# Performance work log

Hardware: AMD Instinct MI355X
Metric: run time of the kernel (lower is better)

## Reference

```python
import jax, jax.numpy as jnp
import numpy as np

B, S, D_IN = 16, 1024, 1024
H, D_OUT = 16, 128

def setup_inputs() -> dict:
    key = jax.random.key(0)
    k1, k2, k3 = jax.random.split(key, 3)
    x = jax.random.normal(k1, (B, S, D_IN), dtype=jnp.float32)
    W = jax.random.normal(k2, (H, 3, D_IN, D_OUT), dtype=jnp.float32) * (1.0 / np.sqrt(D_IN))
    Wo = jax.random.normal(k3, (H * D_OUT, D_OUT), dtype=jnp.float32) * (1.0 / np.sqrt(H * D_OUT))
    return {"x": x, "W": W, "Wo": Wo}

def reference(x, W, Wo):
    # x: [B,S,D_IN], W: [H,3,D_IN,E], Wo: [H*E,E]
    E = W.shape[-1]
    q = jnp.einsum('bsd,hde->bhse', x, W[:, 0])
    k = jnp.einsum('bsd,hde->bhse', x, W[:, 1])
    v = jnp.einsum('bsd,hde->bhse', x, W[:, 2])
    # NOTE: source divides by (output_dim * 0.5), not sqrt(output_dim)
    scores = jnp.einsum('bhse,bhte->bhst', q, k) / (E * 0.5)
    attn = jax.nn.softmax(scores, axis=-1)
    o = jnp.einsum('bhst,bhte->bhse', attn, v)          # [B,H,S,E]
    o = jnp.transpose(o, (0, 2, 1, 3)).reshape(x.shape[0], x.shape[1], -1)  # concat heads
    return jnp.einsum('bsf,fe->bse', o, Wo)
```

## Files before the change

### kernel.cpp

```cpp
#include <hip/hip_runtime.h>

typedef unsigned short u16;
typedef _Float16 f16;
typedef __attribute__((ext_vector_type(8))) _Float16 half8;
typedef __attribute__((ext_vector_type(4))) _Float16 half4;
typedef __attribute__((ext_vector_type(2))) _Float16 half2v;
typedef __attribute__((ext_vector_type(8))) short short8;
typedef __attribute__((ext_vector_type(4))) float f32x4;
typedef __attribute__((ext_vector_type(4))) float f4;
typedef __attribute__((ext_vector_type(4))) u16 u16x4;

#define B_ 16
#define S_ 1024
#define DIN_ 1024
#define H_ 16
#define E_ 128

#define EXPK 0.0225546041776533f

__device__ __forceinline__ u16 f2h(float f) {
  f16 h = (f16)f;
  return __builtin_bit_cast(u16, h);
}

__device__ __forceinline__ half2v pkrtz(float a, float b) {
  return __builtin_bit_cast(half2v, __builtin_amdgcn_cvt_pkrtz(a, b));
}

__device__ __forceinline__ void gl2lds16(const u16* g, u16* l) {
  __builtin_amdgcn_global_load_lds((const __attribute__((address_space(1))) void*)g,
                                   (__attribute__((address_space(3))) void*)l, 16, 0, 0);
}

__global__ __launch_bounds__(256) void zero_f32(float* __restrict__ p) {
  int i = (blockIdx.x * 256 + threadIdx.x) * 4;
  f4 z = {0.f, 0.f, 0.f, 0.f};
  *reinterpret_cast<f4*>(p + i) = z;
}

__global__ __launch_bounds__(256) void cvt_f32_f16(const float* __restrict__ in,
                                                   u16* __restrict__ out) {
  int i = (blockIdx.x * 256 + threadIdx.x) * 4;
  f4 v = *reinterpret_cast<const f4*>(in + i);
  u16x4 o;
  o[0] = f2h(v[0]); o[1] = f2h(v[1]); o[2] = f2h(v[2]); o[3] = f2h(v[3]);
  *reinterpret_cast<u16x4*>(out + i) = o;
}

__global__ __launch_bounds__(256) void transpose_cvt(const float* __restrict__ in,
                                                     u16* __restrict__ out,
                                                     int R, int C) {
  __shared__ float tile[32][33];
  const size_t moff = (size_t)blockIdx.z * R * C;
  const float* src = in + moff;
  u16* dst = out + moff;
  int c0 = blockIdx.x * 32, r0 = blockIdx.y * 32;
  int tx = threadIdx.x & 31, ty = threadIdx.x >> 5;
#pragma unroll
  for (int i = 0; i < 32; i += 8)
    tile[ty + i][tx] = src[(size_t)(r0 + ty + i) * C + c0 + tx];
  __syncthreads();
#pragma unroll
  for (int i = 0; i < 32; i += 8)
    dst[(size_t)(c0 + ty + i) * R + r0 + tx] = f2h(tile[tx][ty + i]);
}

template<int MODE, int KSPLIT, int K>
__global__ __launch_bounds__(256) void gemm_bt(const u16* __restrict__ A,
                                               const u16* __restrict__ BT,
                                               u16* __restrict__ q, u16* __restrict__ kk,
                                               u16* __restrict__ vT, float* __restrict__ out) {
  const int tid = threadIdx.x;
  const int m0 = blockIdx.x * 128;
  const u16* Bblk = BT + (size_t)blockIdx.y * 128 * K;
  __shared__ __align__(16) u16 smem[132 * 128];
  u16* As = smem;
  u16* Bs = smem + 8192;
  const int w = tid >> 6, lane = tid & 63;
  const int quad = lane >> 4, ln = lane & 15;
  const int wr = w >> 1, wc = w & 1;

  const int kbeg = (KSPLIT > 1) ? blockIdx.z * (K / KSPLIT) : 0;
  constexpr int KLEN = K / KSPLIT;

  const int rr = lane >> 3;
  const int cc = (lane & 7) ^ rr;
  const u16* agp[4];
  const u16* bgp[4];
#pragma unroll
  for (int i = 0; i < 4; i++) {
    int row = i * 32 + w * 8 + rr;
    agp[i] = A + (size_t)(m0 + row) * K + kbeg + cc * 8;
    bgp[i] = Bblk + (size_t)row * K + kbeg + cc * 8;
  }

  int offA[4][2], offB[4][2];
#pragma unroll
  for (int mt = 0; mt < 4; mt++) {
    int row = wr * 64 + mt * 16 + ln;
#pragma unroll
    for (int k2 = 0; k2 < 2; k2++)
      offA[mt][k2] = row * 64 + (((k2 * 4 + quad) ^ (ln & 7)) * 8);
  }
#pragma unroll
  for (int nt = 0; nt < 4; nt++) {
    int row = wc * 64 + nt * 16 + ln;
#pragma unroll
    for (int k2 = 0; k2 < 2; k2++)
      offB[nt][k2] = row * 64 + (((k2 * 4 + quad) ^ (ln & 7)) * 8);
  }

  f32x4 acc[4][4];
  f32x4 zero = {0.f, 0.f, 0.f, 0.f};
#pragma unroll
  for (int mt = 0; mt < 4; mt++)
#pragma unroll
    for (int nt = 0; nt < 4; nt++) acc[mt][nt] = zero;

#pragma unroll
  for (int k0 = 0; k0 < KLEN; k0 += 64) {
    __syncthreads();
#pragma unroll
    for (int i = 0; i < 4; i++) {
      gl2lds16(agp[i] + k0, As + i * 2048 + w * 512);
      gl2lds16(bgp[i] + k0, Bs + i * 2048 + w * 512);
    }
    __syncthreads();
#pragma unroll
    for (int k2 = 0; k2 < 2; k2++) {
      half8 af[4], bfr[4];
#pragma unroll
      for (int mt = 0; mt < 4; mt++)
        af[mt] = *reinterpret_cast<const half8*>(&As[offA[mt][k2]]);
#pragma unroll
      for (int nt = 0; nt < 4; nt++)
        bfr[nt] = *reinterpret_cast<const half8*>(&Bs[offB[nt][k2]]);
#pragma unroll
      for (int mt = 0; mt < 4; mt++)
#pragma unroll
        for (int nt = 0; nt < 4; nt++)
          acc[mt][nt] = __builtin_amdgcn_mfma_f32_16x16x32_f16(af[mt], bfr[nt], acc[mt][nt], 0, 0, 0);
    }
  }

  if (MODE == 0) {
    const int h = blockIdx.y / 3, c = blockIdx.y % 3;
    if (c < 2) {
      u16* dst = (c == 0) ? q : kk;
      const float sc = (c == 0) ? EXPK : 1.0f;
#pragma unroll
      for (int mt = 0; mt < 4; mt++)
#pragma unroll
        for (int nt = 0; nt < 4; nt++)
#pragma unroll
          for (int r = 0; r < 4; r++) {
            int row = wr * 64 + mt * 16 + quad * 4 + r;
            int tok = m0 + row;
            int bb = tok >> 10, s = tok & 1023;
            int e = wc * 64 + nt * 16 + ln;
            dst[(((size_t)bb * H_ + h) * S_ + s) * E_ + e] = f2h(acc[mt][nt][r] * sc);
          }
    } else {
      __syncthreads();
#pragma unroll
      for (int mt = 0; mt < 4; mt++)
#pragma unroll
        for (int nt = 0; nt < 4; nt++)
#pragma unroll
          for (int r = 0; r < 4; r++) {
            int row = wr * 64 + mt * 16 + quad * 4 + r;
            int e = wc * 64 + nt * 16 + ln;
            smem[e * 132 + row] = f2h(acc[mt][nt][r]);
          }
      __syncthreads();
      const int bb = m0 >> 10, sbase = m0 & 1023;
      u16* vbase = vT + (((size_t)bb * H_ + h) * E_) * S_;
#pragma unroll
      for (int i = 0; i < 8; i++) {
        int e = (tid >> 4) + i * 16, s0 = (tid & 15) * 8;
        *reinterpret_cast<short8*>(&vbase[(size_t)e * S_ + sbase + s0]) =
            *reinterpret_cast<const short8*>(&smem[e * 132 + s0]);
      }
    }
  } else {
#pragma unroll
    for (int mt = 0; mt < 4; mt++)
#pragma unroll
      for (int nt = 0; nt < 4; nt++)
#pragma unroll
        for (int r = 0; r < 4; r++) {
          int row = wr * 64 + mt * 16 + quad * 4 + r;
          int e = wc * 64 + nt * 16 + ln;
          if (KSPLIT > 1)
            atomicAdd(&out[(size_t)(m0 + row) * E_ + e], acc[mt][nt][r]);
          else
            out[(size_t)(m0 + row) * E_ + e] = acc[mt][nt][r];
        }
  }
}

struct SmemKV {
  u16 ks[64 * 128];
  u16 vs[128 * 64];
};
union SmemAttn {
  u16 qs[128 * 132];
  SmemKV s;
};

__global__ __launch_bounds__(256, 3) void attn_kernel(const u16* __restrict__ qg,
                                                      const u16* __restrict__ kg,
                                                      const u16* __restrict__ vg,
                                                      u16* __restrict__ og) {
  __shared__ __align__(16) SmemAttn sm;
  const int tid = threadIdx.x;
  const int id = blockIdx.x;
  const int g = id >> 6, qt = (id >> 3) & 7, x = id & 7;
  const int hb = g * 8 + x;
  const int b = hb >> 4, h = hb & 15;
  const int q0 = qt * 128;
  const size_t bh = (size_t)(b * H_ + h);
  const u16* qp = qg + bh * S_ * E_;
  const u16* kp = kg + bh * S_ * E_;
  const u16* vp = vg + bh * E_ * S_;
  const int w = tid >> 6, lane = tid & 63, quad = lane >> 4, ln = lane & 15;

#pragma unroll
  for (int i = 0; i < 8; i++) {
    int idx = tid + i * 256;
    int row = idx >> 4, col = (idx & 15) * 8;
    *reinterpret_cast<short8*>(&sm.qs[row * 132 + col]) =
        *reinterpret_cast<const short8*>(&qp[(size_t)(q0 + row) * E_ + col]);
  }
  __syncthreads();
  half8 qf[2][4];
#pragma unroll
  for (int mt = 0; mt < 2; mt++)
#pragma unroll
    for (int ks = 0; ks < 4; ks++)
      qf[mt][ks] = *reinterpret_cast<const half8*>(
          &sm.qs[(w * 32 + mt * 16 + ln) * 132 + ks * 32 + quad * 8]);

  const int krow = w * 4 + (lane >> 4);
  const int kc = ((lane & 15) & 8) | (((lane & 15) & 7) ^ (krow & 7));
  const u16* kbase = kp + (size_t)krow * E_ + kc * 8;
  const int vrow = w * 8 + (lane >> 3);
  const int vc = (lane & 7) ^ ((lane >> 3) & 7);
  const u16* vbase = vp + (size_t)vrow * S_ + vc * 8;

  f32x4 zero = {0.f, 0.f, 0.f, 0.f};
  f32x4 oa[2][8];
#pragma unroll
  for (int mt = 0; mt < 2; mt++)
#pragma unroll
    for (int nt = 0; nt < 8; nt++) oa[mt][nt] = zero;
  float lsum[2] = {0.f, 0.f};

  const int xr = ln & 7, qh = quad >> 1, ql4 = (quad & 1) * 4;

  for (int kt = 0; kt < 16; kt++) {
    __syncthreads();
#pragma unroll
    for (int i = 0; i < 4; i++) {
      gl2lds16(kbase + (size_t)kt * 8192 + i * 16 * E_, &sm.s.ks[(i * 256 + w * 64) * 8]);
      gl2lds16(vbase + (size_t)kt * 64 + i * 32 * S_,   &sm.s.vs[(i * 256 + w * 64) * 8]);
    }
    __syncthreads();

    f32x4 sa[4][2];
#pragma unroll
    for (int t = 0; t < 4; t++)
#pragma unroll
      for (int nt = 0; nt < 2; nt++) sa[t][nt] = zero;
#pragma unroll
    for (int ks = 0; ks < 4; ks++) {
      half8 kf[4];
#pragma unroll
      for (int t = 0; t < 4; t++) {
        int c = ks * 4 + quad;
        int cs = (c & 8) | ((c & 7) ^ xr);
        kf[t] = *reinterpret_cast<const half8*>(&sm.s.ks[(t * 16 + ln) * 128 + cs * 8]);
      }
#pragma unroll
      for (int t = 0; t < 4; t++)
#pragma unroll
        for (int nt = 0; nt < 2; nt++)
          sa[t][nt] = __builtin_amdgcn_mfma_f32_16x16x32_f16(kf[t], qf[nt][ks], sa[t][nt], 0, 0, 0);
    }

    half2v pk[4][2][2];
#pragma unroll
    for (int t = 0; t < 4; t++)
#pragma unroll
      for (int nt = 0; nt < 2; nt++) {
        float p0 = exp2f(sa[t][nt][0]), p1 = exp2f(sa[t][nt][1]);
        float p2 = exp2f(sa[t][nt][2]), p3 = exp2f(sa[t][nt][3]);
        lsum[nt] += (p0 + p1) + (p2 + p3);
        pk[t][nt][0] = pkrtz(p0, p1);
        pk[t][nt][1] = pkrtz(p2, p3);
      }

#pragma unroll
    for (int c2 = 0; c2 < 2; c2++) {
      half8 pf[2];
#pragma unroll
      for (int mt = 0; mt < 2; mt++) {
        union { half8 v8; half2v v2[4]; } u;
        u.v2[0] = pk[2 * c2][mt][0];
        u.v2[1] = pk[2 * c2][mt][1];
        u.v2[2] = pk[2 * c2 + 1][mt][0];
        u.v2[3] = pk[2 * c2 + 1][mt][1];
        pf[mt] = u.v8;
      }
      const int s1 = ((4 * c2 + qh) ^ xr) * 8 + ql4;
      const int s2 = ((4 * c2 + 2 + qh) ^ xr) * 8 + ql4;
#pragma unroll
      for (int nt8 = 0; nt8 < 8; nt8++) {
        int rowoff = (nt8 * 16 + ln) * 64;
        union { half8 v8; half4 h4[2]; } vv;
        vv.h4[0] = *reinterpret_cast<const half4*>(&sm.s.vs[rowoff + s1]);
        vv.h4[1] = *reinterpret_cast<const half4*>(&sm.s.vs[rowoff + s2]);
#pragma unroll
        for (int mt = 0; mt < 2; mt++)
          oa[mt][nt8] = __builtin_amdgcn_mfma_f32_16x16x32_f16(pf[mt], vv.v8, oa[mt][nt8], 0, 0, 0);
      }
    }
  }

  float rl[2];
#pragma unroll
  for (int nt = 0; nt < 2; nt++) {
    float l = lsum[nt];
    l += __shfl_xor(l, 16);
    l += __shfl_xor(l, 32);
    rl[nt] = 1.0f / l;
  }
#pragma unroll
  for (int mt = 0; mt < 2; mt++) {
#pragma unroll
    for (int r = 0; r < 4; r++) {
      int src = (lane & 48) | (quad * 4 + r);
      float rlx = __shfl(rl[mt], src);
      int srow = q0 + w * 32 + mt * 16 + quad * 4 + r;
      size_t base = ((size_t)b * S_ + srow) * (H_ * E_) + (size_t)h * E_;
#pragma unroll
      for (int nt8 = 0; nt8 < 8; nt8++)
        og[base + nt8 * 16 + ln] = f2h(oa[mt][nt8][r] * rlx);
    }
  }
}

extern "C" void kernel_launch(void* const* d_in, const int* in_sizes, int n_in,
                              void* d_out, int out_size, void* d_ws, size_t ws_size,
                              hipStream_t stream) {
  const float* x = (const float*)d_in[0];
  const float* W = (const float*)d_in[1];
  const float* Wo = (const float*)d_in[2];
  float* out = (float*)d_out;
  char* ws = (char*)d_ws;

  const size_t WBT_BYTES = (size_t)H_ * 3 * DIN_ * E_ * 2;
  const size_t WOT_BYTES = (size_t)H_ * E_ * E_ * 2 * 2;
  const size_t FIXED = WBT_BYTES + WOT_BYTES;

  const size_t XB_PER   = (size_t)S_ * DIN_ * 2;
  const size_t QKV_PER  = (size_t)H_ * S_ * E_ * 2;
  const size_t OB_PER   = (size_t)S_ * H_ * E_ * 2;
  const size_t PER_ITEM = XB_PER + 3 * QKV_PER + OB_PER;

  int Bc = 1;
  for (int c = 16; c >= 1; c >>= 1) {
    if (FIXED + (size_t)c * PER_ITEM <= ws_size) { Bc = c; break; }
  }

  u16* WbT = (u16*)(ws);
  u16* WoT = (u16*)(ws + WBT_BYTES);
  char* cb = ws + FIXED;
  u16* xb  = (u16*)(cb);
  u16* qb  = (u16*)(cb + (size_t)Bc * XB_PER);
  u16* kb  = (u16*)(cb + (size_t)Bc * (XB_PER + QKV_PER));
  u16* vTb = (u16*)(cb + (size_t)Bc * (XB_PER + 2 * QKV_PER));
  u16* ob  = (u16*)(cb + (size_t)Bc * (XB_PER + 3 * QKV_PER));

  zero_f32<<<out_size / 1024, 256, 0, stream>>>(out);
  transpose_cvt<<<dim3(4, 32, 48), 256, 0, stream>>>(W, WbT, DIN_, E_);
  transpose_cvt<<<dim3(4, 64, 1), 256, 0, stream>>>(Wo, WoT, H_ * E_, E_);

  for (int b0 = 0; b0 < B_; b0 += Bc) {
    const float* xc = x + (size_t)b0 * S_ * DIN_;
    cvt_f32_f16<<<Bc * S_ * DIN_ / 1024, 256, 0, stream>>>(xc, xb);
    gemm_bt<0, 1, DIN_><<<dim3(Bc * 8, 48), 256, 0, stream>>>(xb, WbT, qb, kb, vTb, nullptr);
    attn_kernel<<<Bc * 128, 256, 0, stream>>>(qb, kb, vTb, ob);
    gemm_bt<1, 4, H_ * E_><<<dim3(Bc * 8, 1, 4), 256, 0, stream>>>(ob, WoT, nullptr, nullptr,
                                                                   nullptr, out + (size_t)b0 * S_ * E_);
  }
}
```

Baseline: 569.2 us.

## Split QKV GEMM into 256x128 tile kernel and shrink attention LDS for occupancy

Replaces the generic gemm_bt with a dedicated QKV projection kernel that uses 256-row tiles, where each wave computes 64x128. This raises reuse of the shared B tile and halves the grid in the M direction, at the cost of more accumulator registers. The attention kernel now loads Q via direct global-to-LDS copies into a swizzled 32KB buffer instead of a padded union, and raises launch bounds from 3 to 4 blocks per CU. The Q epilogue now does a redundant extra store: the unscaled value is written first and then overwritten with the scaled one. The V transpose is done in two halves through shared memory.

Result: slower. 694.5 us (+22.0%).

```diff
diff --git a/kernel.cpp b/kernel.cpp
--- a/kernel.cpp
+++ b/kernel.cpp
@@ -65,22 +65,144 @@
     dst[(size_t)(c0 + ty + i) * R + r0 + tx] = f2h(tile[tx][ty + i]);
 }
 
-template<int MODE, int KSPLIT, int K>
-__global__ __launch_bounds__(256) void gemm_bt(const u16* __restrict__ A,
-                                               const u16* __restrict__ BT,
-                                               u16* __restrict__ q, u16* __restrict__ kk,
-                                               u16* __restrict__ vT, float* __restrict__ out) {
+template<int K>
+__global__ __launch_bounds__(256, 2) void gemm_qkv(const u16* __restrict__ A,
+                                                   const u16* __restrict__ BT,
+                                                   u16* __restrict__ q, u16* __restrict__ kk,
+                                                   u16* __restrict__ vT) {
+  const int tid = threadIdx.x;
+  const int m0 = blockIdx.x * 256;
+  const u16* Bblk = BT + (size_t)blockIdx.y * 128 * K;
+  __shared__ __align__(16) u16 smem[24576];
+  u16* As = smem;
+  u16* Bs = smem + 16384;
+  const int w = tid >> 6, lane = tid & 63;
+  const int quad = lane >> 4, ln = lane & 15;
+
+  const int rr = lane >> 3;
+  const int cc = (lane & 7) ^ rr;
+  const u16* agp[8];
+  const u16* bgp[4];
+#pragma unroll
+  for (int i = 0; i < 8; i++) {
+    int row = i * 32 + w * 8 + rr;
+    agp[i] = A + (size_t)(m0 + row) * K + cc * 8;
+  }
+#pragma unroll
+  for (int i = 0; i < 4; i++) {
+    int row = i * 32 + w * 8 + rr;
+    bgp[i] = Bblk + (size_t)row * K + cc * 8;
+  }
+
+  int offA[4][2], offB[8][2];
+#pragma unroll
+  for (int mt = 0; mt < 4; mt++) {
+    int row = w * 64 + mt * 16 + ln;
+#pragma unroll
+    for (int k2 = 0; k2 < 2; k2++)
+      offA[mt][k2] = row * 64 + (((k2 * 4 + quad) ^ (ln & 7)) * 8);
+  }
+#pragma unroll
+  for (int nt = 0; nt < 8; nt++) {
+    int row = nt * 16 + ln;
+#pragma unroll
+    for (int k2 = 0; k2 < 2; k2++)
+      offB[nt][k2] = row * 64 + (((k2 * 4 + quad) ^ (ln & 7)) * 8);
+  }
+
+  f32x4 acc[4][8];
+  f32x4 zero = {0.f, 0.f, 0.f, 0.f};
+#pragma unroll
+  for (int mt = 0; mt < 4; mt++)
+#pragma unroll
+    for (int nt = 0; nt < 8; nt++) acc[mt][nt] = zero;
+
+#pragma unroll
+  for (int k0 = 0; k0 < K; k0 += 64) {
+    __syncthreads();
+#pragma unroll
+    for (int i = 0; i < 8; i++)
+      gl2lds16(agp[i] + k0, As + i * 2048 + w * 512);
+#pragma unroll
+    for (int i = 0; i < 4; i++)
+      gl2lds16(bgp[i] + k0, Bs + i * 2048 + w * 512);
+    __syncthreads();
+#pragma unroll
+    for (int k2 = 0; k2 < 2; k2++) {
+      half8 af[4], bfr[8];
+#pragma unroll
+      for (int mt = 0; mt < 4; mt++)
+        af[mt] = *reinterpret_cast<const half8*>(&As[offA[mt][k2]]);
+#pragma unroll
+      for (int nt = 0; nt < 8; nt++)
+        bfr[nt] = *reinterpret_cast<const half8*>(&Bs[offB[nt][k2]]);
+#pragma unroll
+      for (int mt = 0; mt < 4; mt++)
+#pragma unroll
+        for (int nt = 0; nt < 8; nt++)
+          acc[mt][nt] = __builtin_amdgcn_mfma_f32_16x16x32_f16(af[mt], bfr[nt], acc[mt][nt], 0, 0, 0);
+    }
+  }
+
+  const int h = blockIdx.y / 3, c = blockIdx.y % 3;
+  if (c < 2) {
+    u16* dst = (c == 0) ? q : kk;
+    const float sc = (c == 0) ? EXPK : 1.0f;
+#pragma unroll
+    for (int mt = 0; mt < 4; mt++)
+#pragma unroll
+      for (int nt = 0; nt < 8; nt++)
+#pragma unroll
+        for (int r = 0; r < 4; r++) {
+          int row = w * 64 + mt * 16 + quad * 4 + r;
+          int tok = m0 + row;
+          int bb = tok >> 10, s = tok & 1023;
+          int e = nt * 16 + ln;
+          dst[(((size_t)bb * H_ + h) * S_ + s) * E_ + e] = f2h(acc[mt][nt][r]);
+          if (c == 0) dst[(((size_t)bb * H_ + h) * S_ + s) * E_ + e] = f2h(acc[mt][nt][r] * sc);
+        }
+  } else {
+    const int bb = m0 >> 10, sbase = m0 & 1023;
+    u16* vbase = vT + (((size_t)bb * H_ + h) * E_) * S_;
+#pragma unroll
+    for (int h2 = 0; h2 < 2; h2++) {
+      __syncthreads();
+      if ((w >> 1) == h2) {
+#pragma unroll
+        for (int mt = 0; mt < 4; mt++)
+#pragma unroll
+          for (int nt = 0; nt < 8; nt++)
+#pragma unroll
+            for (int r = 0; r < 4; r++) {
+              int lr = (w & 1) * 64 + mt * 16 + quad * 4 + r;
+              int e = nt * 16 + ln;
+              smem[e * 132 + lr] = f2h(acc[mt][nt][r]);
+            }
+      }
+      __syncthreads();
+#pragma unroll
+      for (int i = 0; i < 8; i++) {
+        int e = (tid >> 4) + i * 16, s0 = (tid & 15) * 8;
+        *reinterpret_cast<short8*>(&vbase[(size_t)e * S_ + sbase + h2 * 128 + s0]) =
+            *reinterpret_cast<const short8*>(&smem[e * 132 + s0]);
+      }
+    }
+  }
+}
+
+template<int K, int KSPLIT>
+__global__ __launch_bounds__(256) void gemm_out(const u16* __restrict__ A,
+                                                const u16* __restrict__ BT,
+                                                float* __restrict__ out) {
   const int tid = threadIdx.x;
   const int m0 = blockIdx.x * 128;
-  const u16* Bblk = BT + (size_t)blockIdx.y * 128 * K;
-  __shared__ __align__(16) u16 smem[132 * 128];
+  __shared__ __align__(16) u16 smem[16384];
   u16* As = smem;
   u16* Bs = smem + 8192;
   const int w = tid >> 6, lane = tid & 63;
   const int quad = lane >> 4, ln = lane & 15;
   const int wr = w >> 1, wc = w & 1;
-
-  const int kbeg = (KSPLIT > 1) ? blockIdx.z * (K / KSPLIT) : 0;
+  const int kbeg = blockIdx.z * (K / KSPLIT);
   constexpr int KLEN = K / KSPLIT;
 
   const int rr = lane >> 3;
@@ -91,7 +213,7 @@
   for (int i = 0; i < 4; i++) {
     int row = i * 32 + w * 8 + rr;
     agp[i] = A + (size_t)(m0 + row) * K + kbeg + cc * 8;
-    bgp[i] = Bblk + (size_t)row * K + kbeg + cc * 8;
+    bgp[i] = BT + (size_t)row * K + kbeg + cc * 8;
   }
 
   int offA[4][2], offB[4][2];
@@ -143,76 +265,23 @@
     }
   }
 
-  if (MODE == 0) {
-    const int h = blockIdx.y / 3, c = blockIdx.y % 3;
-    if (c < 2) {
-      u16* dst = (c == 0) ? q : kk;
-      const float sc = (c == 0) ? EXPK : 1.0f;
-#pragma unroll
-      for (int mt = 0; mt < 4; mt++)
-#pragma unroll
-        for (int nt = 0; nt < 4; nt++)
-#pragma unroll
-          for (int r = 0; r < 4; r++) {
-            int row = wr * 64 + mt * 16 + quad * 4 + r;
-            int tok = m0 + row;
-            int bb = tok >> 10, s = tok & 1023;
-            int e = wc * 64 + nt * 16 + ln;
-            dst[(((size_t)bb * H_ + h) * S_ + s) * E_ + e] = f2h(acc[mt][nt][r] * sc);
-          }
-    } else {
-      __syncthreads();
-#pragma unroll
-      for (int mt = 0; mt < 4; mt++)
-#pragma unroll
-        for (int nt = 0; nt < 4; nt++)
-#pragma unroll
-          for (int r = 0; r < 4; r++) {
-            int row = wr * 64 + mt * 16 + quad * 4 + r;
-            int e = wc * 64 + nt * 16 + ln;
-            smem[e * 132 + row] = f2h(acc[mt][nt][r]);
-          }
-      __syncthreads();
-      const int bb = m0 >> 10, sbase = m0 & 1023;
-      u16* vbase = vT + (((size_t)bb * H_ + h) * E_) * S_;
-#pragma unroll
-      for (int i = 0; i < 8; i++) {
-        int e = (tid >> 4) + i * 16, s0 = (tid & 15) * 8;
-        *reinterpret_cast<short8*>(&vbase[(size_t)e * S_ + sbase + s0]) =
-            *reinterpret_cast<const short8*>(&smem[e * 132 + s0]);
-      }
-    }
-  } else {
-#pragma unroll
-    for (int mt = 0; mt < 4; mt++)
-#pragma unroll
-      for (int nt = 0; nt < 4; nt++)
-#pragma unroll
-        for (int r = 0; r < 4; r++) {
-          int row = wr * 64 + mt * 16 + quad * 4 + r;
-          int e = wc * 64 + nt * 16 + ln;
-          if (KSPLIT > 1)
-            atomicAdd(&out[(size_t)(m0 + row) * E_ + e], acc[mt][nt][r]);
-          else
-            out[(size_t)(m0 + row) * E_ + e] = acc[mt][nt][r];
-        }
-  }
-}
-
-struct SmemKV {
-  u16 ks[64 * 128];
-  u16 vs[128 * 64];
-};
-union SmemAttn {
-  u16 qs[128 * 132];
-  SmemKV s;
-};
-
-__global__ __launch_bounds__(256, 3) void attn_kernel(const u16* __restrict__ qg,
+#pragma unroll
+  for (int mt = 0; mt < 4; mt++)
+#pragma unroll
+    for (int nt = 0; nt < 4; nt++)
+#pragma unroll
+      for (int r = 0; r < 4; r++) {
+        int row = wr * 64 + mt * 16 + quad * 4 + r;
+        int e = wc * 64 + nt * 16 + ln;
+        atomicAdd(&out[(size_t)(m0 + row) * E_ + e], acc[mt][nt][r]);
+      }
+}
+
+__global__ __launch_bounds__(256, 4) void attn_kernel(const u16* __restrict__ qg,
                                                       const u16* __restrict__ kg,
                                                       const u16* __restrict__ vg,
                                                       u16* __restrict__ og) {
-  __shared__ __align__(16) SmemAttn sm;
+  __shared__ __align__(16) u16 sm[16384];
   const int tid = threadIdx.x;
   const int id = blockIdx.x;
   const int g = id >> 6, qt = (id >> 3) & 7, x = id & 7;
@@ -225,25 +294,23 @@
   const u16* vp = vg + bh * E_ * S_;
   const int w = tid >> 6, lane = tid & 63, quad = lane >> 4, ln = lane & 15;
 
-#pragma unroll
-  for (int i = 0; i < 8; i++) {
-    int idx = tid + i * 256;
-    int row = idx >> 4, col = (idx & 15) * 8;
-    *reinterpret_cast<short8*>(&sm.qs[row * 132 + col]) =
-        *reinterpret_cast<const short8*>(&qp[(size_t)(q0 + row) * E_ + col]);
-  }
+  const int qrow0 = w * 4 + (lane >> 4);
+  const int qc = ((lane & 15) & 8) | (((lane & 15) & 7) ^ (qrow0 & 7));
+#pragma unroll
+  for (int i = 0; i < 8; i++)
+    gl2lds16(qp + (size_t)(q0 + i * 16 + qrow0) * E_ + qc * 8, sm + i * 2048 + w * 512);
   __syncthreads();
   half8 qf[2][4];
 #pragma unroll
   for (int mt = 0; mt < 2; mt++)
 #pragma unroll
-    for (int ks = 0; ks < 4; ks++)
-      qf[mt][ks] = *reinterpret_cast<const half8*>(
-          &sm.qs[(w * 32 + mt * 16 + ln) * 132 + ks * 32 + quad * 8]);
-
-  const int krow = w * 4 + (lane >> 4);
-  const int kc = ((lane & 15) & 8) | (((lane & 15) & 7) ^ (krow & 7));
-  const u16* kbase = kp + (size_t)krow * E_ + kc * 8;
+    for (int ks = 0; ks < 4; ks++) {
+      int c = ks * 4 + quad;
+      int cs = (c & 8) | ((c & 7) ^ (ln & 7));
+      qf[mt][ks] = *reinterpret_cast<const half8*>(&sm[(w * 32 + mt * 16 + ln) * 128 + cs * 8]);
+    }
+
+  const u16* kbase = kp + (size_t)qrow0 * E_ + qc * 8;
   const int vrow = w * 8 + (lane >> 3);
   const int vc = (lane & 7) ^ ((lane >> 3) & 7);
   const u16* vbase = vp + (size_t)vrow * S_ + vc * 8;
@@ -262,8 +329,8 @@
     __syncthreads();
 #pragma unroll
     for (int i = 0; i < 4; i++) {
-      gl2lds16(kbase + (size_t)kt * 8192 + i * 16 * E_, &sm.s.ks[(i * 256 + w * 64) * 8]);
-      gl2lds16(vbase + (size_t)kt * 64 + i * 32 * S_,   &sm.s.vs[(i * 256 + w * 64) * 8]);
+      gl2lds16(kbase + (size_t)kt * 8192 + i * 16 * E_, sm + i * 2048 + w * 512);
+      gl2lds16(vbase + (size_t)kt * 64 + i * 32 * S_,   sm + 8192 + i * 2048 + w * 512);
     }
     __syncthreads();
 
@@ -279,7 +346,7 @@
       for (int t = 0; t < 4; t++) {
         int c = ks * 4 + quad;
         int cs = (c & 8) | ((c & 7) ^ xr);
-        kf[t] = *reinterpret_cast<const half8*>(&sm.s.ks[(t * 16 + ln) * 128 + cs * 8]);
+        kf[t] = *reinterpret_cast<const half8*>(&sm[(t * 16 + ln) * 128 + cs * 8]);
       }
 #pragma unroll
       for (int t = 0; t < 4; t++)
@@ -316,10 +383,10 @@
       const int s2 = ((4 * c2 + 2 + qh) ^ xr) * 8 + ql4;
 #pragma unroll
       for (int nt8 = 0; nt8 < 8; nt8++) {
-        int rowoff = (nt8 * 16 + ln) * 64;
+        int rowoff = 8192 + (nt8 * 16 + ln) * 64;
         union { half8 v8; half4 h4[2]; } vv;
-        vv.h4[0] = *reinterpret_cast<const half4*>(&sm.s.vs[rowoff + s1]);
-        vv.h4[1] = *reinterpret_cast<const half4*>(&sm.s.vs[rowoff + s2]);
+        vv.h4[0] = *reinterpret_cast<const half4*>(&sm[rowoff + s1]);
+        vv.h4[1] = *reinterpret_cast<const half4*>(&sm[rowoff + s2]);
 #pragma unroll
         for (int mt = 0; mt < 2; mt++)
           oa[mt][nt8] = __builtin_amdgcn_mfma_f32_16x16x32_f16(pf[mt], vv.v8, oa[mt][nt8], 0, 0, 0);
@@ -389,9 +456,9 @@
   for (int b0 = 0; b0 < B_; b0 += Bc) {
     const float* xc = x + (size_t)b0 * S_ * DIN_;
     cvt_f32_f16<<<Bc * S_ * DIN_ / 1024, 256, 0, stream>>>(xc, xb);
-    gemm_bt<0, 1, DIN_><<<dim3(Bc * 8, 48), 256, 0, stream>>>(xb, WbT, qb, kb, vTb, nullptr);
+    gemm_qkv<DIN_><<<dim3(Bc * 4, 48), 256, 0, stream>>>(xb, WbT, qb, kb, vTb);
     attn_kernel<<<Bc * 128, 256, 0, stream>>>(qb, kb, vTb, ob);
-    gemm_bt<1, 4, H_ * E_><<<dim3(Bc * 8, 1, 4), 256, 0, stream>>>(ob, WoT, nullptr, nullptr,
-                                                                   nullptr, out + (size_t)b0 * S_ * E_);
-  }
-}
+    gemm_out<H_ * E_, 4><<<dim3(Bc * 8, 1, 4), 256, 0, stream>>>(ob, WoT,
+                                                                 out + (size_t)b0 * S_ * E_);
+  }
+}
```
